# Kernel tuning notes

Hardware: AMD Instinct MI355X
Metric: run time of the kernel (lower is better)

Reference implementation:

```python
import jax, jax.numpy as jnp
import numpy as np

B = 2_000_000
CLAMP_MIN = 0.01
NORM_EPS = 1e-5


def setup_inputs() -> dict:
    key = jax.random.key(0)
    F = jax.random.normal(key, (B, 3, 3), dtype=jnp.float32)
    # learned scalar parameters (per init_kwargs)
    youngs_modulus_log = jnp.asarray(13.0, dtype=jnp.float32)
    poissons_ratio = jnp.asarray(0.3, dtype=jnp.float32)
    yield_stress = jnp.asarray(3000.0, dtype=jnp.float32)
    return {
        "F": F,
        "youngs_modulus_log": youngs_modulus_log,
        "poissons_ratio": poissons_ratio,
        "yield_stress": yield_stress,
    }


def reference(F, youngs_modulus_log, poissons_ratio, yield_stress):
    # von-Mises return mapping on singular values of the deformation gradient
    youngs_modulus = jnp.exp(youngs_modulus_log)
    mu = youngs_modulus / (2.0 * (1.0 + poissons_ratio))  # shear modulus

    # batched 3x3 SVD: U (B,3,3), sigma (B,3), Vh (B,3,3)
    U, sigma, Vh = jnp.linalg.svd(F, full_matrices=False)

    sigma = jnp.maximum(sigma, CLAMP_MIN)
    epsilon = jnp.log(sigma)                                  # (B,3) Hencky strain
    epsilon_trace = jnp.sum(epsilon, axis=1, keepdims=True)   # (B,1)
    epsilon_bar = epsilon - epsilon_trace / 3.0               # deviatoric strain
    epsilon_bar_norm = jnp.linalg.norm(epsilon_bar, axis=1, keepdims=True) + NORM_EPS

    delta_gamma = epsilon_bar_norm - yield_stress / (2.0 * mu)  # (B,1)
    yield_epsilon = epsilon - (delta_gamma / epsilon_bar_norm) * epsilon_bar
    yield_sigma = jnp.exp(yield_epsilon)

    sigma = jnp.where(delta_gamma > 0.0, yield_sigma, sigma)  # (B,3)

    # F_corrected = U @ diag(sigma) @ Vh, fused without materializing diag
    F_corrected = jnp.einsum("bij,bj,bjk->bik", U, sigma, Vh)
    return F_corrected
```

## Files before the change

kernel.cpp:

```cpp
#include <hip/hip_runtime.h>
#include <math.h>

#define TPB 64
#define NQ 2
#define CHUNK (TPB * NQ)
#define CH_F (CHUNK * 9)
#define CH_F4 (CH_F / 4)

typedef float v2  __attribute__((ext_vector_type(2)));
typedef int   v2i __attribute__((ext_vector_type(2)));

static __device__ __forceinline__ v2 V2(float x){ v2 r; r.x=x; r.y=x; return r; }
static __device__ __forceinline__ v2 vfma(v2 a, v2 b, v2 c){ return __builtin_elementwise_fma(a, b, c); }
static __device__ __forceinline__ v2 vmax(v2 a, v2 b){ return __builtin_elementwise_max(a, b); }
static __device__ __forceinline__ v2 vabs(v2 a){ return __builtin_elementwise_abs(a); }
static __device__ __forceinline__ v2 vcps(v2 a, v2 b){ return __builtin_elementwise_copysign(a, b); }

static __device__ __forceinline__ v2 rsq2(v2 x){ v2 r; r.x=__builtin_amdgcn_rsqf(x.x);  r.y=__builtin_amdgcn_rsqf(x.y);  return r; }
static __device__ __forceinline__ v2 rcp2(v2 x){ v2 r; r.x=__builtin_amdgcn_rcpf(x.x);  r.y=__builtin_amdgcn_rcpf(x.y);  return r; }
static __device__ __forceinline__ v2 sqt2(v2 x){ v2 r; r.x=__builtin_amdgcn_sqrtf(x.x); r.y=__builtin_amdgcn_sqrtf(x.y); return r; }
static __device__ __forceinline__ v2 lg22(v2 x){ v2 r; r.x=__builtin_amdgcn_logf(x.x);  r.y=__builtin_amdgcn_logf(x.y);  return r; }
static __device__ __forceinline__ v2 ex22(v2 x){ v2 r; r.x=__builtin_amdgcn_exp2f(x.x); r.y=__builtin_amdgcn_exp2f(x.y); return r; }

static __device__ __forceinline__ v2 vsel(v2i m, v2 a, v2 b){
  v2i ai = __builtin_bit_cast(v2i, a), bi = __builtin_bit_cast(v2i, b);
  return __builtin_bit_cast(v2, bi ^ ((ai ^ bi) & m));
}

__device__ __forceinline__ void jcs2(v2 app_in, v2 aqq_in, v2 apq,
                                     v2& c, v2& s,
                                     v2& app_out, v2& aqq_out)
{
  v2 d    = (aqq_in - app_in) * 0.5f;
  v2 r2   = vmax(vfma(d, d, apq * apq), V2(1e-30f));
  v2 invh = rsq2(r2);
  v2 h    = r2 * invh;
  v2 sg   = vcps(V2(1.0f), d);
  v2 ch   = h + vabs(d);
  v2 sh   = apq * sg;
  v2 w    = rsq2(vfma(ch, ch, sh * sh));
  c = ch * w;
  s = sh * w;
  v2 hs = h * sg;
  v2 m  = app_in + d;
  app_out = m - hs;
  aqq_out = m + hs;
}

__device__ __forceinline__ void jrot(v2& app, v2& aqq, v2& apq,
                                     v2& apk, v2& aqk,
                                     v2& vp0, v2& vp1, v2& vp2,
                                     v2& vq0, v2& vq1, v2& vq2)
{
  v2 c, s;
  jcs2(app, aqq, apq, c, s, app, aqq);
  apq = V2(0.0f);
  v2 pk = apk, qk = aqk;
  apk = c * pk - s * qk;
  aqk = s * pk + c * qk;
  v2 v;
  v = vp0; vp0 = c*v - s*vq0; vq0 = s*v + c*vq0;
  v = vp1; vp1 = c*v - s*vq1; vq1 = s*v + c*vq1;
  v = vp2; vp2 = c*v - s*vq2; vq2 = s*v + c*vq2;
}

#define CSWAP(li, lj, a0, a1, a2, b0, b1, b2)                                   \
  do {                                                                          \
    v2i _m = (li) < (lj);                                                       \
    v2 _t;                                                                      \
    _t = vsel(_m,(lj),(li)); (lj) = vsel(_m,(li),(lj)); (li) = _t;              \
    _t = vsel(_m,(b0),(a0)); (b0) = vsel(_m,(a0),(b0)); (a0) = _t;              \
    _t = vsel(_m,(b1),(a1)); (b1) = vsel(_m,(a1),(b1)); (a1) = _t;              \
    _t = vsel(_m,(b2),(a2)); (b2) = vsel(_m,(a2),(b2)); (a2) = _t;              \
  } while (0)

__global__ __launch_bounds__(TPB) void plastic_svd_kernel(
    const float* __restrict__ F,
    const float* __restrict__ p_yml,
    const float* __restrict__ p_nu,
    const float* __restrict__ p_ys,
    float* __restrict__ out,
    int nmat)
{
  __shared__ float lds[CH_F];
  const int tid = threadIdx.x;
  const int blockBase = blockIdx.x * CHUNK;
  const int gbase = blockBase * 9;
  const int rem = nmat - blockBase;
  const int nfl = (rem >= CHUNK ? CHUNK : rem) * 9;
  const int nfl4 = nfl >> 2;

  {
    const float4* g4 = (const float4*)(F + gbase);
    float4* l4 = (float4*)lds;
    #pragma unroll
    for (int k = 0; k < 5; ++k) {
      int i4 = k * TPB + tid;
      if (i4 < CH_F4 && i4 < nfl4) l4[i4] = g4[i4];
    }
    int i = (nfl & ~3) + tid;
    if (i < nfl) lds[i] = F[gbase + i];
    for (int i2 = nfl + tid; i2 < CH_F; i2 += TPB) lds[i2] = 0.0f;
  }
  __syncthreads();

  const int mi0 = blockBase + tid;
  const int mi1 = blockBase + TPB + tid;
  const float* mA = &lds[tid * 9];
  const float* mB = &lds[(TPB + tid) * 9];

  v2 s00, s11, s22, s01, s02, s12;
  {
    v2 f00,f01,f02,f10,f11,f12,f20,f21,f22;
    f00.x=mA[0]; f01.x=mA[1]; f02.x=mA[2];
    f10.x=mA[3]; f11.x=mA[4]; f12.x=mA[5];
    f20.x=mA[6]; f21.x=mA[7]; f22.x=mA[8];
    f00.y=mB[0]; f01.y=mB[1]; f02.y=mB[2];
    f10.y=mB[3]; f11.y=mB[4]; f12.y=mB[5];
    f20.y=mB[6]; f21.y=mB[7]; f22.y=mB[8];
    s00 = f00*f00 + f10*f10 + f20*f20;
    s11 = f01*f01 + f11*f11 + f21*f21;
    s22 = f02*f02 + f12*f12 + f22*f22;
    s01 = f00*f01 + f10*f11 + f20*f21;
    s02 = f00*f02 + f10*f12 + f20*f22;
    s12 = f01*f02 + f11*f12 + f21*f22;
  }

  const float mu_s = __builtin_amdgcn_exp2f(p_yml[0] * 1.44269504f) *
                     __builtin_amdgcn_rcpf(2.0f * (1.0f + p_nu[0]));
  const float qy_s = p_ys[0] * 0.5f * __builtin_amdgcn_rcpf(mu_s);
  const v2 qy = V2(qy_s);

  v2 v00,v01,v02,v10,v11,v12,v20,v21,v22;
  v2 c, s;

  jcs2(s00, s11, s01, c, s, s00, s11);
  { v2 pk = s02, qk = s12; s02 = c*pk - s*qk; s12 = s*pk + c*qk; }
  v00 = c;  v01 = s;
  v10 = -s; v11 = c;
  s01 = V2(0.0f);
  jcs2(s00, s22, s02, c, s, s00, s22);
  { v2 pk = s01, qk = s12; s01 = c*pk - s*qk; s12 = s*pk + c*qk; }
  v02 = s * v00; v12 = s * v10; v22 = c;
  v00 = c * v00; v10 = c * v10; v20 = -s;
  v21 = V2(0.0f);
  s02 = V2(0.0f);
  jrot(s11, s22, s12, s01, s02, v01, v11, v21, v02, v12, v22);
  jrot(s00, s11, s01, s02, s12, v00, v10, v20, v01, v11, v21);
  jrot(s00, s22, s02, s01, s12, v00, v10, v20, v02, v12, v22);
  jrot(s11, s22, s12, s01, s02, v01, v11, v21, v02, v12, v22);
  jrot(s00, s11, s01, s02, s12, v00, v10, v20, v01, v11, v21);
  jrot(s00, s22, s02, s01, s12, v00, v10, v20, v02, v12, v22);
  jcs2(s11, s22, s12, c, s, s11, s22);
  { v2 v;
    v = v01; v01 = c*v - s*v02; v02 = s*v + c*v02;
    v = v11; v11 = c*v - s*v12; v12 = s*v + c*v12;
    v = v21; v21 = c*v - s*v22; v22 = s*v + c*v22; }

  v2 l0 = s00, l1 = s11, l2 = s22;
  CSWAP(l0, l1, v00, v10, v20, v01, v11, v21);
  CSWAP(l1, l2, v01, v11, v21, v02, v12, v22);
  CSWAP(l0, l1, v00, v10, v20, v01, v11, v21);

  v2 f00,f01,f02,f10,f11,f12,f20,f21,f22;
  f00.x=mA[0]; f01.x=mA[1]; f02.x=mA[2];
  f10.x=mA[3]; f11.x=mA[4]; f12.x=mA[5];
  f20.x=mA[6]; f21.x=mA[7]; f22.x=mA[8];
  f00.y=mB[0]; f01.y=mB[1]; f02.y=mB[2];
  f10.y=mB[3]; f11.y=mB[4]; f12.y=mB[5];
  f20.y=mB[6]; f21.y=mB[7]; f22.y=mB[8];

  v2 w0x = f00*v00 + f01*v10 + f02*v20;
  v2 w0y = f10*v00 + f11*v10 + f12*v20;
  v2 w0z = f20*v00 + f21*v10 + f22*v20;
  v2 n0sq = w0x*w0x + w0y*w0y + w0z*w0z;
  v2 inv0 = rsq2(vmax(n0sq, V2(1e-30f)));
  v2 u0x = w0x*inv0, u0y = w0y*inv0, u0z = w0z*inv0;

  v2 w1x = f00*v01 + f01*v11 + f02*v21;
  v2 w1y = f10*v01 + f11*v11 + f12*v21;
  v2 w1z = f20*v01 + f21*v11 + f22*v21;
  v2 n1sq_pre = w1x*w1x + w1y*w1y + w1z*w1z;
  v2 d01 = w1x*u0x + w1y*u0y + w1z*u0z;
  w1x = w1x - d01*u0x; w1y = w1y - d01*u0y; w1z = w1z - d01*u0z;
  v2 n1sq = w1x*w1x + w1y*w1y + w1z*w1z;
  v2 inv1 = rsq2(vmax(n1sq, V2(1e-30f)));
  v2 u1x = w1x*inv1, u1y = w1y*inv1, u1z = w1z*inv1;

  v2 u2x = u0y*u1z - u0z*u1y;
  v2 u2y = u0z*u1x - u0x*u1z;
  v2 u2z = u0x*u1y - u0y*u1x;
  v2 w2x = f00*v02 + f01*v12 + f02*v22;
  v2 w2y = f10*v02 + f11*v12 + f12*v22;
  v2 w2z = f20*v02 + f21*v12 + f22*v22;
  v2 s2d = u2x*w2x + u2y*w2y + u2z*w2z;
  v2 sg = vcps(V2(1.0f), s2d);
  v2 sig2 = vabs(s2d);
  u2x = u2x * sg; u2y = u2y * sg; u2z = u2z * sg;

  v2 e0 = lg22(vmax(n0sq,     V2(1e-4f))) * 0.5f;
  v2 e1 = lg22(vmax(n1sq_pre, V2(1e-4f))) * 0.5f;
  v2 e2 = lg22(vmax(sig2,     V2(0.01f)));
  v2 m3 = (e0 + e1 + e2) * (1.0f / 3.0f);
  v2 b0 = e0 - m3, b1 = e1 - m3, b2 = e2 - m3;
  v2 bn = sqt2(b0*b0 + b1*b1 + b2*b2) * 0.69314718f + V2(1e-5f);
  v2 r = vmax(bn - qy, V2(0.0f)) * rcp2(bn);
  v2 c0 = ex22(e0 - r * b0);
  v2 c1 = ex22(e1 - r * b1);
  v2 c2 = ex22(e2 - r * b2);

  v2 a0x = c0*u0x, a0y = c0*u0y, a0z = c0*u0z;
  v2 a1x = c1*u1x, a1y = c1*u1y, a1z = c1*u1z;
  v2 a2x = c2*u2x, a2y = c2*u2y, a2z = c2*u2z;

  v2 o00 = a0x*v00 + a1x*v01 + a2x*v02;
  v2 o01 = a0x*v10 + a1x*v11 + a2x*v12;
  v2 o02 = a0x*v20 + a1x*v21 + a2x*v22;
  v2 o10 = a0y*v00 + a1y*v01 + a2y*v02;
  v2 o11 = a0y*v10 + a1y*v11 + a2y*v12;
  v2 o12 = a0y*v20 + a1y*v21 + a2y*v22;
  v2 o20 = a0z*v00 + a1z*v01 + a2z*v02;
  v2 o21 = a0z*v10 + a1z*v11 + a2z*v12;
  v2 o22 = a0z*v20 + a1z*v21 + a2z*v22;

  if (mi0 < nmat) {
    float* m = &lds[tid * 9];
    m[0]=o00.x; m[1]=o01.x; m[2]=o02.x;
    m[3]=o10.x; m[4]=o11.x; m[5]=o12.x;
    m[6]=o20.x; m[7]=o21.x; m[8]=o22.x;
  }
  if (mi1 < nmat) {
    float* m = &lds[(TPB + tid) * 9];
    m[0]=o00.y; m[1]=o01.y; m[2]=o02.y;
    m[3]=o10.y; m[4]=o11.y; m[5]=o12.y;
    m[6]=o20.y; m[7]=o21.y; m[8]=o22.y;
  }
  __syncthreads();

  {
    float4* g4 = (float4*)(out + gbase);
    const float4* l4 = (const float4*)lds;
    #pragma unroll
    for (int k = 0; k < 5; ++k) {
      int i4 = k * TPB + tid;
      if (i4 < CH_F4 && i4 < nfl4) g4[i4] = l4[i4];
    }
    int i = (nfl & ~3) + tid;
    if (i < nfl) out[gbase + i] = lds[i];
  }
}

extern "C" void kernel_launch(void* const* d_in, const int* in_sizes, int n_in,
                              void* d_out, int out_size, void* d_ws, size_t ws_size,
                              hipStream_t stream) {
  const float* F     = (const float*)d_in[0];
  const float* p_yml = (const float*)d_in[1];
  const float* p_nu  = (const float*)d_in[2];
  const float* p_ys  = (const float*)d_in[3];
  float* out = (float*)d_out;

  const int nmat = in_sizes[0] / 9;
  const int nblocks = (nmat + CHUNK - 1) / CHUNK;
  hipLaunchKernelGGL(plastic_svd_kernel, dim3(nblocks), dim3(TPB), 0, stream,
                     F, p_yml, p_nu, p_ys, out, nmat);
}
```

Baseline: 33.36 us.

## Make kernel persistent with double-buffered async global-to-LDS prefetch

The kernel becomes a grid-stride persistent loop over chunks, launched with at most 4096 blocks. While the current chunk is being computed, the next chunk's matrices are prefetched straight into a second LDS buffer using global_load_lds. The barrier before the store-back is replaced by a per-wave lgkmcnt wait, which is sound only because each block is a single 64-lane wavefront. The goal is to hide global load latency behind the SVD math and cut block launch overhead. The cost is doubled LDS use per block and fewer blocks to spread across the GPU.

```diff
diff --git a/kernel.cpp b/kernel.cpp
--- a/kernel.cpp
+++ b/kernel.cpp
@@ -25,6 +25,17 @@
 static __device__ __forceinline__ v2 vsel(v2i m, v2 a, v2 b){
   v2i ai = __builtin_bit_cast(v2i, a), bi = __builtin_bit_cast(v2i, b);
   return __builtin_bit_cast(v2, bi ^ ((ai ^ bi) & m));
+}
+
+static __device__ __forceinline__ void gl_lds16(const float* g, float* l){
+  __builtin_amdgcn_global_load_lds(
+      (const __attribute__((address_space(1))) void*)g,
+      (__attribute__((address_space(3))) void*)l, 16, 0, 0);
+}
+
+static __device__ __forceinline__ void lds_fence(){
+  asm volatile("s_waitcnt lgkmcnt(0)" ::: "memory");
+  __builtin_amdgcn_sched_barrier(0);
 }
 
 __device__ __forceinline__ void jcs2(v2 app_in, v2 aqq_in, v2 apq,
@@ -80,37 +91,98 @@
     const float* __restrict__ p_nu,
     const float* __restrict__ p_ys,
     float* __restrict__ out,
-    int nmat)
+    int nmat, int nchunks)
 {
-  __shared__ float lds[CH_F];
+  __shared__ float lds[2][CH_F];
   const int tid = threadIdx.x;
-  const int blockBase = blockIdx.x * CHUNK;
-  const int gbase = blockBase * 9;
-  const int rem = nmat - blockBase;
-  const int nfl = (rem >= CHUNK ? CHUNK : rem) * 9;
-  const int nfl4 = nfl >> 2;
-
-  {
-    const float4* g4 = (const float4*)(F + gbase);
-    float4* l4 = (float4*)lds;
+
+  const float mu_s = __builtin_amdgcn_exp2f(p_yml[0] * 1.44269504f) *
+                     __builtin_amdgcn_rcpf(2.0f * (1.0f + p_nu[0]));
+  const float qy_s = p_ys[0] * 0.5f * __builtin_amdgcn_rcpf(mu_s);
+  const v2 qy = V2(qy_s);
+
+  auto STAGE = [&](int t, int b){
+    const int fbase = t * CH_F;
+    const int rem = nmat - t * CHUNK;
+    const int nfl = (rem >= CHUNK ? CHUNK : rem) * 9;
+    const int nfl4 = nfl >> 2;
+    const float4* g4 = (const float4*)(F + fbase);
     #pragma unroll
     for (int k = 0; k < 5; ++k) {
       int i4 = k * TPB + tid;
-      if (i4 < CH_F4 && i4 < nfl4) l4[i4] = g4[i4];
+      if (i4 < CH_F4 && i4 < nfl4)
+        gl_lds16((const float*)(g4 + i4), &lds[b][i4 * 4]);
     }
     int i = (nfl & ~3) + tid;
-    if (i < nfl) lds[i] = F[gbase + i];
-    for (int i2 = nfl + tid; i2 < CH_F; i2 += TPB) lds[i2] = 0.0f;
-  }
-  __syncthreads();
-
-  const int mi0 = blockBase + tid;
-  const int mi1 = blockBase + TPB + tid;
-  const float* mA = &lds[tid * 9];
-  const float* mB = &lds[(TPB + tid) * 9];
-
-  v2 s00, s11, s22, s01, s02, s12;
-  {
+    if (i < nfl) lds[b][i] = F[fbase + i];
+    for (int i2 = nfl + tid; i2 < CH_F; i2 += TPB) lds[b][i2] = 0.0f;
+  };
+
+  int cur = 0;
+  const int t0 = blockIdx.x;
+  if (t0 < nchunks) STAGE(t0, 0);
+
+  for (int t = t0; t < nchunks; t += gridDim.x) {
+    __syncthreads();
+    const int tn = t + gridDim.x;
+    if (tn < nchunks) STAGE(tn, cur ^ 1);
+
+    const int blockBase = t * CHUNK;
+    const int gbase = blockBase * 9;
+    const int mi0 = blockBase + tid;
+    const int mi1 = blockBase + TPB + tid;
+    float* bufc = lds[cur];
+    const float* mA = &bufc[tid * 9];
+    const float* mB = &bufc[(TPB + tid) * 9];
+
+    v2 s00, s11, s22, s01, s02, s12;
+    {
+      v2 f00,f01,f02,f10,f11,f12,f20,f21,f22;
+      f00.x=mA[0]; f01.x=mA[1]; f02.x=mA[2];
+      f10.x=mA[3]; f11.x=mA[4]; f12.x=mA[5];
+      f20.x=mA[6]; f21.x=mA[7]; f22.x=mA[8];
+      f00.y=mB[0]; f01.y=mB[1]; f02.y=mB[2];
+      f10.y=mB[3]; f11.y=mB[4]; f12.y=mB[5];
+      f20.y=mB[6]; f21.y=mB[7]; f22.y=mB[8];
+      s00 = f00*f00 + f10*f10 + f20*f20;
+      s11 = f01*f01 + f11*f11 + f21*f21;
+      s22 = f02*f02 + f12*f12 + f22*f22;
+      s01 = f00*f01 + f10*f11 + f20*f21;
+      s02 = f00*f02 + f10*f12 + f20*f22;
+      s12 = f01*f02 + f11*f12 + f21*f22;
+    }
+
+    v2 v00,v01,v02,v10,v11,v12,v20,v21,v22;
+    v2 c, s;
+
+    jcs2(s00, s11, s01, c, s, s00, s11);
+    { v2 pk = s02, qk = s12; s02 = c*pk - s*qk; s12 = s*pk + c*qk; }
+    v00 = c;  v01 = s;
+    v10 = -s; v11 = c;
+    s01 = V2(0.0f);
+    jcs2(s00, s22, s02, c, s, s00, s22);
+    { v2 pk = s01, qk = s12; s01 = c*pk - s*qk; s12 = s*pk + c*qk; }
+    v02 = s * v00; v12 = s * v10; v22 = c;
+    v00 = c * v00; v10 = c * v10; v20 = -s;
+    v21 = V2(0.0f);
+    s02 = V2(0.0f);
+    jrot(s11, s22, s12, s01, s02, v01, v11, v21, v02, v12, v22);
+    jrot(s00, s11, s01, s02, s12, v00, v10, v20, v01, v11, v21);
+    jrot(s00, s22, s02, s01, s12, v00, v10, v20, v02, v12, v22);
+    jrot(s11, s22, s12, s01, s02, v01, v11, v21, v02, v12, v22);
+    jrot(s00, s11, s01, s02, s12, v00, v10, v20, v01, v11, v21);
+    jrot(s00, s22, s02, s01, s12, v00, v10, v20, v02, v12, v22);
+    jcs2(s11, s22, s12, c, s, s11, s22);
+    { v2 v;
+      v = v01; v01 = c*v - s*v02; v02 = s*v + c*v02;
+      v = v11; v11 = c*v - s*v12; v12 = s*v + c*v12;
+      v = v21; v21 = c*v - s*v22; v22 = s*v + c*v22; }
+
+    v2 l0 = s00, l1 = s11, l2 = s22;
+    CSWAP(l0, l1, v00, v10, v20, v01, v11, v21);
+    CSWAP(l1, l2, v01, v11, v21, v02, v12, v22);
+    CSWAP(l0, l1, v00, v10, v20, v01, v11, v21);
+
     v2 f00,f01,f02,f10,f11,f12,f20,f21,f22;
     f00.x=mA[0]; f01.x=mA[1]; f02.x=mA[2];
     f10.x=mA[3]; f11.x=mA[4]; f12.x=mA[5];
@@ -118,135 +190,89 @@
     f00.y=mB[0]; f01.y=mB[1]; f02.y=mB[2];
     f10.y=mB[3]; f11.y=mB[4]; f12.y=mB[5];
     f20.y=mB[6]; f21.y=mB[7]; f22.y=mB[8];
-    s00 = f00*f00 + f10*f10 + f20*f20;
-    s11 = f01*f01 + f11*f11 + f21*f21;
-    s22 = f02*f02 + f12*f12 + f22*f22;
-    s01 = f00*f01 + f10*f11 + f20*f21;
-    s02 = f00*f02 + f10*f12 + f20*f22;
-    s12 = f01*f02 + f11*f12 + f21*f22;
-  }
-
-  const float mu_s = __builtin_amdgcn_exp2f(p_yml[0] * 1.44269504f) *
-                     __builtin_amdgcn_rcpf(2.0f * (1.0f + p_nu[0]));
-  const float qy_s = p_ys[0] * 0.5f * __builtin_amdgcn_rcpf(mu_s);
-  const v2 qy = V2(qy_s);
-
-  v2 v00,v01,v02,v10,v11,v12,v20,v21,v22;
-  v2 c, s;
-
-  jcs2(s00, s11, s01, c, s, s00, s11);
-  { v2 pk = s02, qk = s12; s02 = c*pk - s*qk; s12 = s*pk + c*qk; }
-  v00 = c;  v01 = s;
-  v10 = -s; v11 = c;
-  s01 = V2(0.0f);
-  jcs2(s00, s22, s02, c, s, s00, s22);
-  { v2 pk = s01, qk = s12; s01 = c*pk - s*qk; s12 = s*pk + c*qk; }
-  v02 = s * v00; v12 = s * v10; v22 = c;
-  v00 = c * v00; v10 = c * v10; v20 = -s;
-  v21 = V2(0.0f);
-  s02 = V2(0.0f);
-  jrot(s11, s22, s12, s01, s02, v01, v11, v21, v02, v12, v22);
-  jrot(s00, s11, s01, s02, s12, v00, v10, v20, v01, v11, v21);
-  jrot(s00, s22, s02, s01, s12, v00, v10, v20, v02, v12, v22);
-  jrot(s11, s22, s12, s01, s02, v01, v11, v21, v02, v12, v22);
-  jrot(s00, s11, s01, s02, s12, v00, v10, v20, v01, v11, v21);
-  jrot(s00, s22, s02, s01, s12, v00, v10, v20, v02, v12, v22);
-  jcs2(s11, s22, s12, c, s, s11, s22);
-  { v2 v;
-    v = v01; v01 = c*v - s*v02; v02 = s*v + c*v02;
-    v = v11; v11 = c*v - s*v12; v12 = s*v + c*v12;
-    v = v21; v21 = c*v - s*v22; v22 = s*v + c*v22; }
-
-  v2 l0 = s00, l1 = s11, l2 = s22;
-  CSWAP(l0, l1, v00, v10, v20, v01, v11, v21);
-  CSWAP(l1, l2, v01, v11, v21, v02, v12, v22);
-  CSWAP(l0, l1, v00, v10, v20, v01, v11, v21);
-
-  v2 f00,f01,f02,f10,f11,f12,f20,f21,f22;
-  f00.x=mA[0]; f01.x=mA[1]; f02.x=mA[2];
-  f10.x=mA[3]; f11.x=mA[4]; f12.x=mA[5];
-  f20.x=mA[6]; f21.x=mA[7]; f22.x=mA[8];
-  f00.y=mB[0]; f01.y=mB[1]; f02.y=mB[2];
-  f10.y=mB[3]; f11.y=mB[4]; f12.y=mB[5];
-  f20.y=mB[6]; f21.y=mB[7]; f22.y=mB[8];
-
-  v2 w0x = f00*v00 + f01*v10 + f02*v20;
-  v2 w0y = f10*v00 + f11*v10 + f12*v20;
-  v2 w0z = f20*v00 + f21*v10 + f22*v20;
-  v2 n0sq = w0x*w0x + w0y*w0y + w0z*w0z;
-  v2 inv0 = rsq2(vmax(n0sq, V2(1e-30f)));
-  v2 u0x = w0x*inv0, u0y = w0y*inv0, u0z = w0z*inv0;
-
-  v2 w1x = f00*v01 + f01*v11 + f02*v21;
-  v2 w1y = f10*v01 + f11*v11 + f12*v21;
-  v2 w1z = f20*v01 + f21*v11 + f22*v21;
-  v2 n1sq_pre = w1x*w1x + w1y*w1y + w1z*w1z;
-  v2 d01 = w1x*u0x + w1y*u0y + w1z*u0z;
-  w1x = w1x - d01*u0x; w1y = w1y - d01*u0y; w1z = w1z - d01*u0z;
-  v2 n1sq = w1x*w1x + w1y*w1y + w1z*w1z;
-  v2 inv1 = rsq2(vmax(n1sq, V2(1e-30f)));
-  v2 u1x = w1x*inv1, u1y = w1y*inv1, u1z = w1z*inv1;
-
-  v2 u2x = u0y*u1z - u0z*u1y;
-  v2 u2y = u0z*u1x - u0x*u1z;
-  v2 u2z = u0x*u1y - u0y*u1x;
-  v2 w2x = f00*v02 + f01*v12 + f02*v22;
-  v2 w2y = f10*v02 + f11*v12 + f12*v22;
-  v2 w2z = f20*v02 + f21*v12 + f22*v22;
-  v2 s2d = u2x*w2x + u2y*w2y + u2z*w2z;
-  v2 sg = vcps(V2(1.0f), s2d);
-  v2 sig2 = vabs(s2d);
-  u2x = u2x * sg; u2y = u2y * sg; u2z = u2z * sg;
-
-  v2 e0 = lg22(vmax(n0sq,     V2(1e-4f))) * 0.5f;
-  v2 e1 = lg22(vmax(n1sq_pre, V2(1e-4f))) * 0.5f;
-  v2 e2 = lg22(vmax(sig2,     V2(0.01f)));
-  v2 m3 = (e0 + e1 + e2) * (1.0f / 3.0f);
-  v2 b0 = e0 - m3, b1 = e1 - m3, b2 = e2 - m3;
-  v2 bn = sqt2(b0*b0 + b1*b1 + b2*b2) * 0.69314718f + V2(1e-5f);
-  v2 r = vmax(bn - qy, V2(0.0f)) * rcp2(bn);
-  v2 c0 = ex22(e0 - r * b0);
-  v2 c1 = ex22(e1 - r * b1);
-  v2 c2 = ex22(e2 - r * b2);
-
-  v2 a0x = c0*u0x, a0y = c0*u0y, a0z = c0*u0z;
-  v2 a1x = c1*u1x, a1y = c1*u1y, a1z = c1*u1z;
-  v2 a2x = c2*u2x, a2y = c2*u2y, a2z = c2*u2z;
-
-  v2 o00 = a0x*v00 + a1x*v01 + a2x*v02;
-  v2 o01 = a0x*v10 + a1x*v11 + a2x*v12;
-  v2 o02 = a0x*v20 + a1x*v21 + a2x*v22;
-  v2 o10 = a0y*v00 + a1y*v01 + a2y*v02;
-  v2 o11 = a0y*v10 + a1y*v11 + a2y*v12;
-  v2 o12 = a0y*v20 + a1y*v21 + a2y*v22;
-  v2 o20 = a0z*v00 + a1z*v01 + a2z*v02;
-  v2 o21 = a0z*v10 + a1z*v11 + a2z*v12;
-  v2 o22 = a0z*v20 + a1z*v21 + a2z*v22;
-
-  if (mi0 < nmat) {
-    float* m = &lds[tid * 9];
-    m[0]=o00.x; m[1]=o01.x; m[2]=o02.x;
-    m[3]=o10.x; m[4]=o11.x; m[5]=o12.x;
-    m[6]=o20.x; m[7]=o21.x; m[8]=o22.x;
-  }
-  if (mi1 < nmat) {
-    float* m = &lds[(TPB + tid) * 9];
-    m[0]=o00.y; m[1]=o01.y; m[2]=o02.y;
-    m[3]=o10.y; m[4]=o11.y; m[5]=o12.y;
-    m[6]=o20.y; m[7]=o21.y; m[8]=o22.y;
-  }
-  __syncthreads();
-
-  {
-    float4* g4 = (float4*)(out + gbase);
-    const float4* l4 = (const float4*)lds;
-    #pragma unroll
-    for (int k = 0; k < 5; ++k) {
-      int i4 = k * TPB + tid;
-      if (i4 < CH_F4 && i4 < nfl4) g4[i4] = l4[i4];
-    }
-    int i = (nfl & ~3) + tid;
-    if (i < nfl) out[gbase + i] = lds[i];
+
+    v2 w0x = f00*v00 + f01*v10 + f02*v20;
+    v2 w0y = f10*v00 + f11*v10 + f12*v20;
+    v2 w0z = f20*v00 + f21*v10 + f22*v20;
+    v2 n0sq = w0x*w0x + w0y*w0y + w0z*w0z;
+    v2 inv0 = rsq2(vmax(n0sq, V2(1e-30f)));
+    v2 u0x = w0x*inv0, u0y = w0y*inv0, u0z = w0z*inv0;
+
+    v2 w1x = f00*v01 + f01*v11 + f02*v21;
+    v2 w1y = f10*v01 + f11*v11 + f12*v21;
+    v2 w1z = f20*v01 + f21*v11 + f22*v21;
+    v2 n1sq_pre = w1x*w1x + w1y*w1y + w1z*w1z;
+    v2 d01 = w1x*u0x + w1y*u0y + w1z*u0z;
+    w1x = w1x - d01*u0x; w1y = w1y - d01*u0y; w1z = w1z - d01*u0z;
+    v2 n1sq = w1x*w1x + w1y*w1y + w1z*w1z;
+    v2 inv1 = rsq2(vmax(n1sq, V2(1e-30f)));
+    v2 u1x = w1x*inv1, u1y = w1y*inv1, u1z = w1z*inv1;
+
+    v2 u2x = u0y*u1z - u0z*u1y;
+    v2 u2y = u0z*u1x - u0x*u1z;
+    v2 u2z = u0x*u1y - u0y*u1x;
+    v2 w2x = f00*v02 + f01*v12 + f02*v22;
+    v2 w2y = f10*v02 + f11*v12 + f12*v22;
+    v2 w2z = f20*v02 + f21*v12 + f22*v22;
+    v2 s2d = u2x*w2x + u2y*w2y + u2z*w2z;
+    v2 sg = vcps(V2(1.0f), s2d);
+    v2 sig2 = vabs(s2d);
+    u2x = u2x * sg; u2y = u2y * sg; u2z = u2z * sg;
+
+    v2 e0 = lg22(vmax(n0sq,     V2(1e-4f))) * 0.5f;
+    v2 e1 = lg22(vmax(n1sq_pre, V2(1e-4f))) * 0.5f;
+    v2 e2 = lg22(vmax(sig2,     V2(0.01f)));
+    v2 m3 = (e0 + e1 + e2) * (1.0f / 3.0f);
+    v2 b0 = e0 - m3, b1 = e1 - m3, b2 = e2 - m3;
+    v2 bn = sqt2(b0*b0 + b1*b1 + b2*b2) * 0.69314718f + V2(1e-5f);
+    v2 r = vmax(bn - qy, V2(0.0f)) * rcp2(bn);
+    v2 c0 = ex22(e0 - r * b0);
+    v2 c1 = ex22(e1 - r * b1);
+    v2 c2 = ex22(e2 - r * b2);
+
+    v2 a0x = c0*u0x, a0y = c0*u0y, a0z = c0*u0z;
+    v2 a1x = c1*u1x, a1y = c1*u1y, a1z = c1*u1z;
+    v2 a2x = c2*u2x, a2y = c2*u2y, a2z = c2*u2z;
+
+    v2 o00 = a0x*v00 + a1x*v01 + a2x*v02;
+    v2 o01 = a0x*v10 + a1x*v11 + a2x*v12;
+    v2 o02 = a0x*v20 + a1x*v21 + a2x*v22;
+    v2 o10 = a0y*v00 + a1y*v01 + a2y*v02;
+    v2 o11 = a0y*v10 + a1y*v11 + a2y*v12;
+    v2 o12 = a0y*v20 + a1y*v21 + a2y*v22;
+    v2 o20 = a0z*v00 + a1z*v01 + a2z*v02;
+    v2 o21 = a0z*v10 + a1z*v11 + a2z*v12;
+    v2 o22 = a0z*v20 + a1z*v21 + a2z*v22;
+
+    if (mi0 < nmat) {
+      float* m = &bufc[tid * 9];
+      m[0]=o00.x; m[1]=o01.x; m[2]=o02.x;
+      m[3]=o10.x; m[4]=o11.x; m[5]=o12.x;
+      m[6]=o20.x; m[7]=o21.x; m[8]=o22.x;
+    }
+    if (mi1 < nmat) {
+      float* m = &bufc[(TPB + tid) * 9];
+      m[0]=o00.y; m[1]=o01.y; m[2]=o02.y;
+      m[3]=o10.y; m[4]=o11.y; m[5]=o12.y;
+      m[6]=o20.y; m[7]=o21.y; m[8]=o22.y;
+    }
+    lds_fence();
+
+    {
+      const int rem = nmat - blockBase;
+      const int nfl = (rem >= CHUNK ? CHUNK : rem) * 9;
+      const int nfl4 = nfl >> 2;
+      float4* g4 = (float4*)(out + gbase);
+      const float4* l4 = (const float4*)bufc;
+      #pragma unroll
+      for (int k = 0; k < 5; ++k) {
+        int i4 = k * TPB + tid;
+        if (i4 < CH_F4 && i4 < nfl4) g4[i4] = l4[i4];
+      }
+      int i = (nfl & ~3) + tid;
+      if (i < nfl) out[gbase + i] = bufc[i];
+    }
+    cur ^= 1;
   }
 }
 
@@ -260,7 +286,9 @@
   float* out = (float*)d_out;
 
   const int nmat = in_sizes[0] / 9;
-  const int nblocks = (nmat + CHUNK - 1) / CHUNK;
-  hipLaunchKernelGGL(plastic_svd_kernel, dim3(nblocks), dim3(TPB), 0, stream,
-                     F, p_yml, p_nu, p_ys, out, nmat);
-}
+  const int nchunks = (nmat + CHUNK - 1) / CHUNK;
+  int G = 16 * 256;
+  if (G > nchunks) G = nchunks;
+  hipLaunchKernelGGL(plastic_svd_kernel, dim3(G), dim3(TPB), 0, stream,
+                     F, p_yml, p_nu, p_ys, out, nmat, nchunks);
+}
```

Result: slower. 35.92 us (+7.7%).

## Process four chunks per block with register prefetch and double-buffered LDS

Applied to the files above, without the earlier changes.

Each block now loops over four consecutive chunks instead of one. It prefetches the next chunk's global data into registers while computing the current chunk, then stages it into a second LDS buffer. The block is a single wavefront, so __syncthreads is replaced by an lgkmcnt wait plus a scheduler barrier. The intent is to hide global load latency and cut launch and block overhead, at the cost of more registers, a quarter as many blocks, and less wave-level parallelism across the GPU.

```diff
diff --git a/kernel.cpp b/kernel.cpp
--- a/kernel.cpp
+++ b/kernel.cpp
@@ -6,6 +6,7 @@
 #define CHUNK (TPB * NQ)
 #define CH_F (CHUNK * 9)
 #define CH_F4 (CH_F / 4)
+#define NCH 4
 
 typedef float v2  __attribute__((ext_vector_type(2)));
 typedef int   v2i __attribute__((ext_vector_type(2)));
@@ -25,6 +26,11 @@
 static __device__ __forceinline__ v2 vsel(v2i m, v2 a, v2 b){
   v2i ai = __builtin_bit_cast(v2i, a), bi = __builtin_bit_cast(v2i, b);
   return __builtin_bit_cast(v2, bi ^ ((ai ^ bi) & m));
+}
+
+static __device__ __forceinline__ void lds_fence(){
+  asm volatile("s_waitcnt lgkmcnt(0)" ::: "memory");
+  __builtin_amdgcn_sched_barrier(0);
 }
 
 __device__ __forceinline__ void jcs2(v2 app_in, v2 aqq_in, v2 apq,
@@ -82,35 +88,116 @@
     float* __restrict__ out,
     int nmat)
 {
-  __shared__ float lds[CH_F];
+  __shared__ float lds[2][CH_F];
   const int tid = threadIdx.x;
-  const int blockBase = blockIdx.x * CHUNK;
-  const int gbase = blockBase * 9;
-  const int rem = nmat - blockBase;
-  const int nfl = (rem >= CHUNK ? CHUNK : rem) * 9;
-  const int nfl4 = nfl >> 2;
-
-  {
-    const float4* g4 = (const float4*)(F + gbase);
-    float4* l4 = (float4*)lds;
+  const int c0  = blockIdx.x * NCH;
+
+  const float mu_s = __builtin_amdgcn_exp2f(p_yml[0] * 1.44269504f) *
+                     __builtin_amdgcn_rcpf(2.0f * (1.0f + p_nu[0]));
+  const float qy_s = p_ys[0] * 0.5f * __builtin_amdgcn_rcpf(mu_s);
+  const v2 qy = V2(qy_s);
+
+  auto LOADS = [&](int c, float4* r, float& tail){
+    const int rem = nmat - c * CHUNK;
+    const int nn  = rem >= CHUNK ? CHUNK : rem;
+    const int nfl = nn * 9, nfl4 = nfl >> 2;
+    const float4* g4 = (const float4*)F + (size_t)c * CH_F4;
     #pragma unroll
     for (int k = 0; k < 5; ++k) {
       int i4 = k * TPB + tid;
-      if (i4 < CH_F4 && i4 < nfl4) l4[i4] = g4[i4];
-    }
-    int i = (nfl & ~3) + tid;
-    if (i < nfl) lds[i] = F[gbase + i];
-    for (int i2 = nfl + tid; i2 < CH_F; i2 += TPB) lds[i2] = 0.0f;
-  }
-  __syncthreads();
-
-  const int mi0 = blockBase + tid;
-  const int mi1 = blockBase + TPB + tid;
-  const float* mA = &lds[tid * 9];
-  const float* mB = &lds[(TPB + tid) * 9];
-
-  v2 s00, s11, s22, s01, s02, s12;
-  {
+      r[k] = make_float4(0.f, 0.f, 0.f, 0.f);
+      if (i4 < nfl4) r[k] = g4[i4];
+    }
+    tail = 0.f;
+    int e = (nfl & ~3) + tid;
+    if (e < nfl) tail = F[(size_t)c * CH_F + e];
+  };
+
+  auto STAGEW = [&](int c, int b, const float4* r, float tail){
+    const int rem = nmat - c * CHUNK;
+    const int nn  = rem >= CHUNK ? CHUNK : rem;
+    const int nfl = nn * 9;
+    float4* l4 = (float4*)lds[b];
+    #pragma unroll
+    for (int k = 0; k < 5; ++k) {
+      int i4 = k * TPB + tid;
+      if (i4 < CH_F4) l4[i4] = r[k];
+    }
+    int e = (nfl & ~3) + tid;
+    if (e < nfl) lds[b][e] = tail;
+  };
+
+  float4 A[5]; float tA;
+  LOADS(c0, A, tA);
+  STAGEW(c0, 0, A, tA);
+  lds_fence();
+
+  for (int j = 0; j < NCH; ++j) {
+    const int c = c0 + j;
+    const int blockBase = c * CHUNK;
+    if (blockBase >= nmat) break;
+    const int b = j & 1;
+    const bool more = (j + 1 < NCH) && ((c + 1) * CHUNK < nmat);
+    if (more) LOADS(c + 1, A, tA);
+
+    const int gbase = blockBase * 9;
+    const int rem = nmat - blockBase;
+    const int nfl = (rem >= CHUNK ? CHUNK : rem) * 9;
+    const int nfl4 = nfl >> 2;
+    const int mi0 = blockBase + tid;
+    const int mi1 = blockBase + TPB + tid;
+    float* bufc = lds[b];
+    const float* mA = &bufc[tid * 9];
+    const float* mB = &bufc[(TPB + tid) * 9];
+
+    v2 s00, s11, s22, s01, s02, s12;
+    {
+      v2 f00,f01,f02,f10,f11,f12,f20,f21,f22;
+      f00.x=mA[0]; f01.x=mA[1]; f02.x=mA[2];
+      f10.x=mA[3]; f11.x=mA[4]; f12.x=mA[5];
+      f20.x=mA[6]; f21.x=mA[7]; f22.x=mA[8];
+      f00.y=mB[0]; f01.y=mB[1]; f02.y=mB[2];
+      f10.y=mB[3]; f11.y=mB[4]; f12.y=mB[5];
+      f20.y=mB[6]; f21.y=mB[7]; f22.y=mB[8];
+      s00 = f00*f00 + f10*f10 + f20*f20;
+      s11 = f01*f01 + f11*f11 + f21*f21;
+      s22 = f02*f02 + f12*f12 + f22*f22;
+      s01 = f00*f01 + f10*f11 + f20*f21;
+      s02 = f00*f02 + f10*f12 + f20*f22;
+      s12 = f01*f02 + f11*f12 + f21*f22;
+    }
+
+    v2 v00,v01,v02,v10,v11,v12,v20,v21,v22;
+    v2 c_, s_;
+
+    jcs2(s00, s11, s01, c_, s_, s00, s11);
+    { v2 pk = s02, qk = s12; s02 = c_*pk - s_*qk; s12 = s_*pk + c_*qk; }
+    v00 = c_;  v01 = s_;
+    v10 = -s_; v11 = c_;
+    s01 = V2(0.0f);
+    jcs2(s00, s22, s02, c_, s_, s00, s22);
+    { v2 pk = s01, qk = s12; s01 = c_*pk - s_*qk; s12 = s_*pk + c_*qk; }
+    v02 = s_ * v00; v12 = s_ * v10; v22 = c_;
+    v00 = c_ * v00; v10 = c_ * v10; v20 = -s_;
+    v21 = V2(0.0f);
+    s02 = V2(0.0f);
+    jrot(s11, s22, s12, s01, s02, v01, v11, v21, v02, v12, v22);
+    jrot(s00, s11, s01, s02, s12, v00, v10, v20, v01, v11, v21);
+    jrot(s00, s22, s02, s01, s12, v00, v10, v20, v02, v12, v22);
+    jrot(s11, s22, s12, s01, s02, v01, v11, v21, v02, v12, v22);
+    jrot(s00, s11, s01, s02, s12, v00, v10, v20, v01, v11, v21);
+    jrot(s00, s22, s02, s01, s12, v00, v10, v20, v02, v12, v22);
+    jcs2(s11, s22, s12, c_, s_, s11, s22);
+    { v2 v;
+      v = v01; v01 = c_*v - s_*v02; v02 = s_*v + c_*v02;
+      v = v11; v11 = c_*v - s_*v12; v12 = s_*v + c_*v12;
+      v = v21; v21 = c_*v - s_*v22; v22 = s_*v + c_*v22; }
+
+    v2 l0 = s00, l1 = s11, l2 = s22;
+    CSWAP(l0, l1, v00, v10, v20, v01, v11, v21);
+    CSWAP(l1, l2, v01, v11, v21, v02, v12, v22);
+    CSWAP(l0, l1, v00, v10, v20, v01, v11, v21);
+
     v2 f00,f01,f02,f10,f11,f12,f20,f21,f22;
     f00.x=mA[0]; f01.x=mA[1]; f02.x=mA[2];
     f10.x=mA[3]; f11.x=mA[4]; f12.x=mA[5];
@@ -118,135 +205,91 @@
     f00.y=mB[0]; f01.y=mB[1]; f02.y=mB[2];
     f10.y=mB[3]; f11.y=mB[4]; f12.y=mB[5];
     f20.y=mB[6]; f21.y=mB[7]; f22.y=mB[8];
-    s00 = f00*f00 + f10*f10 + f20*f20;
-    s11 = f01*f01 + f11*f11 + f21*f21;
-    s22 = f02*f02 + f12*f12 + f22*f22;
-    s01 = f00*f01 + f10*f11 + f20*f21;
-    s02 = f00*f02 + f10*f12 + f20*f22;
-    s12 = f01*f02 + f11*f12 + f21*f22;
-  }
-
-  const float mu_s = __builtin_amdgcn_exp2f(p_yml[0] * 1.44269504f) *
-                     __builtin_amdgcn_rcpf(2.0f * (1.0f + p_nu[0]));
-  const float qy_s = p_ys[0] * 0.5f * __builtin_amdgcn_rcpf(mu_s);
-  const v2 qy = V2(qy_s);
-
-  v2 v00,v01,v02,v10,v11,v12,v20,v21,v22;
-  v2 c, s;
-
-  jcs2(s00, s11, s01, c, s, s00, s11);
-  { v2 pk = s02, qk = s12; s02 = c*pk - s*qk; s12 = s*pk + c*qk; }
-  v00 = c;  v01 = s;
-  v10 = -s; v11 = c;
-  s01 = V2(0.0f);
-  jcs2(s00, s22, s02, c, s, s00, s22);
-  { v2 pk = s01, qk = s12; s01 = c*pk - s*qk; s12 = s*pk + c*qk; }
-  v02 = s * v00; v12 = s * v10; v22 = c;
-  v00 = c * v00; v10 = c * v10; v20 = -s;
-  v21 = V2(0.0f);
-  s02 = V2(0.0f);
-  jrot(s11, s22, s12, s01, s02, v01, v11, v21, v02, v12, v22);
-  jrot(s00, s11, s01, s02, s12, v00, v10, v20, v01, v11, v21);
-  jrot(s00, s22, s02, s01, s12, v00, v10, v20, v02, v12, v22);
-  jrot(s11, s22, s12, s01, s02, v01, v11, v21, v02, v12, v22);
-  jrot(s00, s11, s01, s02, s12, v00, v10, v20, v01, v11, v21);
-  jrot(s00, s22, s02, s01, s12, v00, v10, v20, v02, v12, v22);
-  jcs2(s11, s22, s12, c, s, s11, s22);
-  { v2 v;
-    v = v01; v01 = c*v - s*v02; v02 = s*v + c*v02;
-    v = v11; v11 = c*v - s*v12; v12 = s*v + c*v12;
-    v = v21; v21 = c*v - s*v22; v22 = s*v + c*v22; }
-
-  v2 l0 = s00, l1 = s11, l2 = s22;
-  CSWAP(l0, l1, v00, v10, v20, v01, v11, v21);
-  CSWAP(l1, l2, v01, v11, v21, v02, v12, v22);
-  CSWAP(l0, l1, v00, v10, v20, v01, v11, v21);
-
-  v2 f00,f01,f02,f10,f11,f12,f20,f21,f22;
-  f00.x=mA[0]; f01.x=mA[1]; f02.x=mA[2];
-  f10.x=mA[3]; f11.x=mA[4]; f12.x=mA[5];
-  f20.x=mA[6]; f21.x=mA[7]; f22.x=mA[8];
-  f00.y=mB[0]; f01.y=mB[1]; f02.y=mB[2];
-  f10.y=mB[3]; f11.y=mB[4]; f12.y=mB[5];
-  f20.y=mB[6]; f21.y=mB[7]; f22.y=mB[8];
-
-  v2 w0x = f00*v00 + f01*v10 + f02*v20;
-  v2 w0y = f10*v00 + f11*v10 + f12*v20;
-  v2 w0z = f20*v00 + f21*v10 + f22*v20;
-  v2 n0sq = w0x*w0x + w0y*w0y + w0z*w0z;
-  v2 inv0 = rsq2(vmax(n0sq, V2(1e-30f)));
-  v2 u0x = w0x*inv0, u0y = w0y*inv0, u0z = w0z*inv0;
-
-  v2 w1x = f00*v01 + f01*v11 + f02*v21;
-  v2 w1y = f10*v01 + f11*v11 + f12*v21;
-  v2 w1z = f20*v01 + f21*v11 + f22*v21;
-  v2 n1sq_pre = w1x*w1x + w1y*w1y + w1z*w1z;
-  v2 d01 = w1x*u0x + w1y*u0y + w1z*u0z;
-  w1x = w1x - d01*u0x; w1y = w1y - d01*u0y; w1z = w1z - d01*u0z;
-  v2 n1sq = w1x*w1x + w1y*w1y + w1z*w1z;
-  v2 inv1 = rsq2(vmax(n1sq, V2(1e-30f)));
-  v2 u1x = w1x*inv1, u1y = w1y*inv1, u1z = w1z*inv1;
-
-  v2 u2x = u0y*u1z - u0z*u1y;
-  v2 u2y = u0z*u1x - u0x*u1z;
-  v2 u2z = u0x*u1y - u0y*u1x;
-  v2 w2x = f00*v02 + f01*v12 + f02*v22;
-  v2 w2y = f10*v02 + f11*v12 + f12*v22;
-  v2 w2z = f20*v02 + f21*v12 + f22*v22;
-  v2 s2d = u2x*w2x + u2y*w2y + u2z*w2z;
-  v2 sg = vcps(V2(1.0f), s2d);
-  v2 sig2 = vabs(s2d);
-  u2x = u2x * sg; u2y = u2y * sg; u2z = u2z * sg;
-
-  v2 e0 = lg22(vmax(n0sq,     V2(1e-4f))) * 0.5f;
-  v2 e1 = lg22(vmax(n1sq_pre, V2(1e-4f))) * 0.5f;
-  v2 e2 = lg22(vmax(sig2,     V2(0.01f)));
-  v2 m3 = (e0 + e1 + e2) * (1.0f / 3.0f);
-  v2 b0 = e0 - m3, b1 = e1 - m3, b2 = e2 - m3;
-  v2 bn = sqt2(b0*b0 + b1*b1 + b2*b2) * 0.69314718f + V2(1e-5f);
-  v2 r = vmax(bn - qy, V2(0.0f)) * rcp2(bn);
-  v2 c0 = ex22(e0 - r * b0);
-  v2 c1 = ex22(e1 - r * b1);
-  v2 c2 = ex22(e2 - r * b2);
-
-  v2 a0x = c0*u0x, a0y = c0*u0y, a0z = c0*u0z;
-  v2 a1x = c1*u1x, a1y = c1*u1y, a1z = c1*u1z;
-  v2 a2x = c2*u2x, a2y = c2*u2y, a2z = c2*u2z;
-
-  v2 o00 = a0x*v00 + a1x*v01 + a2x*v02;
-  v2 o01 = a0x*v10 + a1x*v11 + a2x*v12;
-  v2 o02 = a0x*v20 + a1x*v21 + a2x*v22;
-  v2 o10 = a0y*v00 + a1y*v01 + a2y*v02;
-  v2 o11 = a0y*v10 + a1y*v11 + a2y*v12;
-  v2 o12 = a0y*v20 + a1y*v21 + a2y*v22;
-  v2 o20 = a0z*v00 + a1z*v01 + a2z*v02;
-  v2 o21 = a0z*v10 + a1z*v11 + a2z*v12;
-  v2 o22 = a0z*v20 + a1z*v21 + a2z*v22;
-
-  if (mi0 < nmat) {
-    float* m = &lds[tid * 9];
-    m[0]=o00.x; m[1]=o01.x; m[2]=o02.x;
-    m[3]=o10.x; m[4]=o11.x; m[5]=o12.x;
-    m[6]=o20.x; m[7]=o21.x; m[8]=o22.x;
-  }
-  if (mi1 < nmat) {
-    float* m = &lds[(TPB + tid) * 9];
-    m[0]=o00.y; m[1]=o01.y; m[2]=o02.y;
-    m[3]=o10.y; m[4]=o11.y; m[5]=o12.y;
-    m[6]=o20.y; m[7]=o21.y; m[8]=o22.y;
-  }
-  __syncthreads();
-
-  {
-    float4* g4 = (float4*)(out + gbase);
-    const float4* l4 = (const float4*)lds;
-    #pragma unroll
-    for (int k = 0; k < 5; ++k) {
-      int i4 = k * TPB + tid;
-      if (i4 < CH_F4 && i4 < nfl4) g4[i4] = l4[i4];
-    }
-    int i = (nfl & ~3) + tid;
-    if (i < nfl) out[gbase + i] = lds[i];
+
+    v2 w0x = f00*v00 + f01*v10 + f02*v20;
+    v2 w0y = f10*v00 + f11*v10 + f12*v20;
+    v2 w0z = f20*v00 + f21*v10 + f22*v20;
+    v2 n0sq = w0x*w0x + w0y*w0y + w0z*w0z;
+    v2 inv0 = rsq2(vmax(n0sq, V2(1e-30f)));
+    v2 u0x = w0x*inv0, u0y = w0y*inv0, u0z = w0z*inv0;
+
+    v2 w1x = f00*v01 + f01*v11 + f02*v21;
+    v2 w1y = f10*v01 + f11*v11 + f12*v21;
+    v2 w1z = f20*v01 + f21*v11 + f22*v21;
+    v2 n1sq_pre = w1x*w1x + w1y*w1y + w1z*w1z;
+    v2 d01 = w1x*u0x + w1y*u0y + w1z*u0z;
+    w1x = w1x - d01*u0x; w1y = w1y - d01*u0y; w1z = w1z - d01*u0z;
+    v2 n1sq = w1x*w1x + w1y*w1y + w1z*w1z;
+    v2 inv1 = rsq2(vmax(n1sq, V2(1e-30f)));
+    v2 u1x = w1x*inv1, u1y = w1y*inv1, u1z = w1z*inv1;
+
+    v2 u2x = u0y*u1z - u0z*u1y;
+    v2 u2y = u0z*u1x - u0x*u1z;
+    v2 u2z = u0x*u1y - u0y*u1x;
+    v2 w2x = f00*v02 + f01*v12 + f02*v22;
+    v2 w2y = f10*v02 + f11*v12 + f12*v22;
+    v2 w2z = f20*v02 + f21*v12 + f22*v22;
+    v2 s2d = u2x*w2x + u2y*w2y + u2z*w2z;
+    v2 sg = vcps(V2(1.0f), s2d);
+    v2 sig2 = vabs(s2d);
+    u2x = u2x * sg; u2y = u2y * sg; u2z = u2z * sg;
+
+    v2 e0 = lg22(vmax(n0sq,     V2(1e-4f))) * 0.5f;
+    v2 e1 = lg22(vmax(n1sq_pre, V2(1e-4f))) * 0.5f;
+    v2 e2 = lg22(vmax(sig2,     V2(0.01f)));
+    v2 m3 = (e0 + e1 + e2) * (1.0f / 3.0f);
+    v2 b0 = e0 - m3, b1 = e1 - m3, b2 = e2 - m3;
+    v2 bn = sqt2(b0*b0 + b1*b1 + b2*b2) * 0.69314718f + V2(1e-5f);
+    v2 r = vmax(bn - qy, V2(0.0f)) * rcp2(bn);
+    v2 c0v = ex22(e0 - r * b0);
+    v2 c1v = ex22(e1 - r * b1);
+    v2 c2v = ex22(e2 - r * b2);
+
+    v2 a0x = c0v*u0x, a0y = c0v*u0y, a0z = c0v*u0z;
+    v2 a1x = c1v*u1x, a1y = c1v*u1y, a1z = c1v*u1z;
+    v2 a2x = c2v*u2x, a2y = c2v*u2y, a2z = c2v*u2z;
+
+    v2 o00 = a0x*v00 + a1x*v01 + a2x*v02;
+    v2 o01 = a0x*v10 + a1x*v11 + a2x*v12;
+    v2 o02 = a0x*v20 + a1x*v21 + a2x*v22;
+    v2 o10 = a0y*v00 + a1y*v01 + a2y*v02;
+    v2 o11 = a0y*v10 + a1y*v11 + a2y*v12;
+    v2 o12 = a0y*v20 + a1y*v21 + a2y*v22;
+    v2 o20 = a0z*v00 + a1z*v01 + a2z*v02;
+    v2 o21 = a0z*v10 + a1z*v01*0.0f + a1z*v11 + a2z*v12 - a1z*v01*0.0f;
+    v2 o22 = a0z*v20 + a1z*v21 + a2z*v22;
+    o21 = a0z*v10 + a1z*v11 + a2z*v12;
+
+    if (mi0 < nmat) {
+      float* m = &bufc[tid * 9];
+      m[0]=o00.x; m[1]=o01.x; m[2]=o02.x;
+      m[3]=o10.x; m[4]=o11.x; m[5]=o12.x;
+      m[6]=o20.x; m[7]=o21.x; m[8]=o22.x;
+    }
+    if (mi1 < nmat) {
+      float* m = &bufc[(TPB + tid) * 9];
+      m[0]=o00.y; m[1]=o01.y; m[2]=o02.y;
+      m[3]=o10.y; m[4]=o11.y; m[5]=o12.y;
+      m[6]=o20.y; m[7]=o21.y; m[8]=o22.y;
+    }
+    lds_fence();
+
+    {
+      float4* g4 = (float4*)(out + gbase);
+      const float4* l4 = (const float4*)bufc;
+      #pragma unroll
+      for (int k = 0; k < 5; ++k) {
+        int i4 = k * TPB + tid;
+        if (i4 < nfl4) g4[i4] = l4[i4];
+      }
+      int e = (nfl & ~3) + tid;
+      if (e < nfl) out[gbase + e] = bufc[e];
+    }
+
+    if (more) {
+      STAGEW(c + 1, b ^ 1, A, tA);
+      lds_fence();
+    }
   }
 }
 
@@ -260,7 +303,7 @@
   float* out = (float*)d_out;
 
   const int nmat = in_sizes[0] / 9;
-  const int nblocks = (nmat + CHUNK - 1) / CHUNK;
+  const int nblocks = (nmat + CHUNK * NCH - 1) / (CHUNK * NCH);
   hipLaunchKernelGGL(plastic_svd_kernel, dim3(nblocks), dim3(TPB), 0, stream,
                      F, p_yml, p_nu, p_ys, out, nmat);
 }
```

Measured after the change: 35.07 us. 5.1% more time.
